# Optimization experiments

Measured on AMD Instinct MI355X. Metric: run time of the kernel, lower is better.

The kernel has to match this reference:

```python
import jax, jax.numpy as jnp
import numpy as np

START_LABEL_ID = 4  # tag_to_ix['[CLS]']


def setup_inputs() -> dict:
    key = jax.random.key(0)
    k1, k2 = jax.random.split(key)
    B, T, K = 256, 4096, 6
    feats = jax.random.normal(k1, (B, T, K), dtype=jnp.float32)
    transitions = jax.random.normal(k2, (B, T, K, K), dtype=jnp.float32)
    return {"feats": feats, "transitions": transitions}


def reference(feats, transitions):
    # Viterbi decode (Bert_BiLSTM_CRF._viterbi_decode):
    #   log_delta init -10000 except start tag; per step t:
    #     scores   = transitions[:, t] + log_delta[:, None, :]   # [B, K, K]
    #     log_delta = max_k scores + feats[:, t]
    #     psi[:, t] = argmax_k scores  (backpointers)
    B, T, K = feats.shape
    init = jnp.full((B, K), -10000.0, dtype=feats.dtype).at[:, START_LABEL_ID].set(0.0)

    def step(delta, xs):
        trans_t, feat_t = xs                       # [B,K,K], [B,K]
        scores = trans_t + delta[:, None, :]       # [B,K,K]
        new_delta = jnp.max(scores, axis=-1) + feat_t
        psi_t = jnp.argmax(scores, axis=-1)        # [B,K] backpointers
        return new_delta, psi_t

    # time-major xs for scan over t = 1..T-1
    xs = (jnp.swapaxes(transitions[:, 1:], 0, 1),  # [T-1,B,K,K]
          jnp.swapaxes(feats[:, 1:], 0, 1))        # [T-1,B,K]
    final_delta, psis = jax.lax.scan(step, init, xs)  # psis: [T-1,B,K]

    score = jnp.max(final_delta, axis=-1)              # [B]
    last_tag = jnp.argmax(final_delta, axis=-1)        # [B]

    # Backtrack: path[t] = psi[t+1][path[t+1]]; psis[i] is psi at time i+1,
    # so path[t] = gather(psis[t], path[t+1]) for t = T-2 .. 0.
    def back(next_tag, psi_t):
        tag = jnp.take_along_axis(psi_t, next_tag[:, None], axis=-1)[:, 0]
        return tag, tag

    _, tags = jax.lax.scan(back, last_tag, psis, reverse=True)  # tags[i] = path[i], i=0..T-2
    path = jnp.concatenate([tags, last_tag[None, :]], axis=0).T  # [B,T]
    return score, path
```

## Files before the change

### kernel.cpp

```cpp
#include <hip/hip_runtime.h>

#define NB 256
#define NT 4096
#define CH 128
#define NCHUNK (NT / CH)

typedef unsigned int u32;
typedef unsigned long long u64;
typedef int v2i __attribute__((ext_vector_type(2)));

typedef __attribute__((address_space(1))) const u32 gas_u32;
typedef __attribute__((address_space(3))) u32 las_u32;

__device__ __forceinline__ void gll16(const void* g, void* l) {
  __builtin_amdgcn_global_load_lds((gas_u32*)g, (las_u32*)l, 16, 0, 0);
}

template <int CTRL>
__device__ __forceinline__ float dppf(float x) {
  return __int_as_float(__builtin_amdgcn_update_dpp(
      0, __float_as_int(x), CTRL, 0xF, 0xF, true));
}

__device__ __forceinline__ float pl16max(float x) {
#if __has_builtin(__builtin_amdgcn_permlane16_swap)
  v2i r = __builtin_amdgcn_permlane16_swap(__float_as_int(x), __float_as_int(x),
                                           false, false);
  return fmaxf(__int_as_float(r[0]), __int_as_float(r[1]));
#else
  return fmaxf(x, __shfl_xor(x, 16, 64));
#endif
}

__device__ __forceinline__ float pl32max(float x) {
#if __has_builtin(__builtin_amdgcn_permlane32_swap)
  v2i r = __builtin_amdgcn_permlane32_swap(__float_as_int(x), __float_as_int(x),
                                           false, false);
  return fmaxf(__int_as_float(r[0]), __int_as_float(r[1]));
#else
  return fmaxf(x, __shfl_xor(x, 32, 64));
#endif
}

__global__ void __launch_bounds__(64, 1)
viterbi_k(const float* __restrict__ feats, const float* __restrict__ trans,
          float* __restrict__ out) {
  __shared__ __align__(16) float s_tr[2 * CH * 36];
  __shared__ __align__(16) float s_ft[2 * CH * 6];
  __shared__ u32 s_psi[NT];
  __shared__ u32 s_path[NT / 4];

  const int b = blockIdx.x;
  const int lane = (int)threadIdx.x;
  const int g = lane >> 3;
  const int l = lane & 7;
  const int gg = (g < 6) ? g : 5;
  const int jj = (l < 6) ? l : 5;
  const int offTA = gg * 6 + jj;
  const int offTB = jj * 6 + gg;
  const int offFA = gg;
  const int offFB = jj;

  const float* trb = trans + (size_t)b * NT * 36;
  const float* ftb = feats + (size_t)b * NT * 6;

  float delta = (l == 4) ? 0.0f : -10000.0f;
  u32 mlo = 0, mhi = 0;

  auto stage = [&](int c) {
    const int buf = c & 1;
    const float* gt = trb + (size_t)c * CH * 36;
    float* lt = s_tr + buf * (CH * 36);
#pragma unroll
    for (int i = 0; i < 18; ++i) gll16(gt + i * 256 + lane * 4, lt + i * 256);
    const float* gf = ftb + (size_t)c * CH * 6;
    float* lf = s_ft + buf * (CH * 6);
#pragma unroll
    for (int i = 0; i < 3; ++i) gll16(gf + i * 256 + lane * 4, lf + i * 256);
  };

  auto stepA = [&](float tr, float ft, int slot) {
    float s = tr + delta;
    float m = fmaxf(s, dppf<0xB1>(s));
    m = fmaxf(m, dppf<0x4E>(m));
    m = fmaxf(m, dppf<0x141>(m));
    u64 bal = __ballot(s == m);
    bool cap = (lane == slot);
    mlo = cap ? (u32)bal : mlo;
    mhi = cap ? (u32)(bal >> 32) : mhi;
    delta = m + ft;
  };

  auto stepB = [&](float tr, float ft, int slot) {
    float s = tr + delta;
    float m = fmaxf(s, dppf<0x128>(s));
    m = pl16max(m);
    m = pl32max(m);
    u64 bal = __ballot(s == m);
    bool cap = (lane == slot);
    mlo = cap ? (u32)bal : mlo;
    mhi = cap ? (u32)(bal >> 32) : mhi;
    delta = m + ft;
  };

  auto flush = [&](int base) {
    const u32 ub = (u32)(base >> 6) & 63;
    u32 pA = (u32)__builtin_ctz((mlo & 63u) | 64u);
    pA |= (u32)__builtin_ctz(((mlo >> 8) & 63u) | 64u) << 3;
    pA |= (u32)__builtin_ctz(((mlo >> 16) & 63u) | 64u) << 6;
    pA |= (u32)__builtin_ctz(((mlo >> 24) & 63u) | 64u) << 9;
    pA |= (u32)__builtin_ctz((mhi & 63u) | 64u) << 12;
    pA |= (u32)__builtin_ctz(((mhi >> 8) & 63u) | 64u) << 15;
    u64 bal = ((u64)mhi << 32) | (u64)mlo;
    u32 pB = 0;
#pragma unroll
    for (int i = 0; i < 6; ++i) {
      u64 mm = (bal >> i) & 0x0000010101010101ULL;
      u32 j = (u32)(__builtin_ctzll(mm | (1ULL << 48)) >> 3);
      pB |= j << (3 * i);
    }
    u32 p = (lane & 1) ? pA : pB;
    s_psi[base + (((u32)lane) ^ ub)] = p;
  };

#define LOAD8(trv, ftv, g8base)                                               \
  {                                                                           \
    _Pragma("unroll") for (int q = 0; q < 8; ++q) {                           \
      trv[q] = trp[((g8base) + q) * 36 + ((q & 1) ? offTA : offTB)];          \
      ftv[q] = ftp[((g8base) + q) * 6 + ((q & 1) ? offFA : offFB)];           \
    }                                                                         \
  }

#define STEPS8(trv, ftv, base)                                                \
  {                                                                           \
    _Pragma("unroll") for (int q = 0; q < 8; ++q) {                           \
      if (q & 1) stepA(trv[q], ftv[q], ((base) + q) & 63);                    \
      else       stepB(trv[q], ftv[q], ((base) + q) & 63);                    \
    }                                                                         \
  }

  stage(0);
  asm volatile("s_waitcnt vmcnt(0)" ::: "memory");
  stage(1);

  {
    const float* trp = s_tr;
    const float* ftp = s_ft;
    float trA[8], ftA[8], trB[8], ftB[8];
    LOAD8(trA, ftA, 0);
    LOAD8(trB, ftB, 8);
#pragma unroll
    for (int q = 1; q < 8; ++q) {
      if (q & 1) stepA(trA[q], ftA[q], q);
      else       stepB(trA[q], ftA[q], q);
    }
    LOAD8(trA, ftA, 16);
    STEPS8(trB, ftB, 8);
#pragma unroll 1
    for (int g2 = 2; g2 < 16; g2 += 2) {
      LOAD8(trB, ftB, (g2 + 1) * 8);
      STEPS8(trA, ftA, g2 * 8);
      LOAD8(trA, ftA, (g2 + 2) * 8);
      STEPS8(trB, ftB, (g2 + 1) * 8);
      if ((g2 & 7) == 6) flush((g2 & 8) * 8);
    }
  }

#pragma unroll 1
  for (int c = 1; c < NCHUNK; ++c) {
    asm volatile("s_waitcnt vmcnt(0)" ::: "memory");
    if (c + 1 < NCHUNK) stage(c + 1);
    const int buf = c & 1;
    const float* trp = s_tr + buf * (CH * 36);
    const float* ftp = s_ft + buf * (CH * 6);
    const int tbase = c * CH;
    float trA[8], ftA[8], trB[8], ftB[8];
    LOAD8(trA, ftA, 0);
#pragma unroll 1
    for (int g2 = 0; g2 < 16; g2 += 2) {
      LOAD8(trB, ftB, (g2 + 1) * 8);
      STEPS8(trA, ftA, tbase + g2 * 8);
      LOAD8(trA, ftA, (g2 + 2) * 8);
      STEPS8(trB, ftB, tbase + (g2 + 1) * 8);
      if ((g2 & 7) == 6) flush(tbase + (g2 & 8) * 8);
    }
  }

  float sm = delta;
  sm = fmaxf(sm, dppf<0xB1>(sm));
  sm = fmaxf(sm, dppf<0x4E>(sm));
  sm = fmaxf(sm, dppf<0x141>(sm));
  sm = fmaxf(sm, dppf<0x128>(sm));
  sm = pl16max(sm);
  sm = pl32max(sm);
  u64 bs = __ballot(delta == sm);
  int last_tag = (int)((__builtin_ctzll(bs) >> 3) & 7);

  __syncthreads();

  const int u = lane;
  u32 Gm = 0u | (1u << 3) | (2u << 6) | (3u << 9) | (4u << 12) | (5u << 15);
#pragma unroll 1
  for (int k = 0; k < 64; ++k) {
    u32 p = s_psi[u * 64 + (k ^ u)];
    u32 ng = 0;
#pragma unroll
    for (int x = 0; x < 6; ++x) {
      u32 j = (p >> (3 * x)) & 7;
      u32 v = (Gm >> (3 * ((j < 6) ? j : 0))) & 7;
      ng |= v << (3 * x);
    }
    Gm = ng;
  }

  int bcur = last_tag;
  int my_b = last_tag;
#pragma unroll 1
  for (int v = 63; v >= 1; --v) {
    u32 Gv = (u32)__builtin_amdgcn_readlane((int)Gm, v);
    bcur = (int)((Gv >> (3 * bcur)) & 7);
    my_b = (u == v - 1) ? bcur : my_b;
  }

  {
    int tag = my_b;
    unsigned char* pb = (unsigned char*)s_path;
    pb[u * 64 + 63] = (unsigned char)tag;
#pragma unroll 1
    for (int k = 63; k >= 1; --k) {
      u32 p = s_psi[u * 64 + (k ^ u)];
      tag = (int)((p >> (3 * tag)) & 7);
      pb[u * 64 + k - 1] = (unsigned char)tag;
    }
  }
  if (lane == 0) out[b] = sm;
  __syncthreads();

  float* outp = out + NB + (size_t)b * NT;
#pragma unroll
  for (int i = 0; i < (NT / 4) / 64; ++i) {
    u32 w = s_path[lane + i * 64];
    float4 f;
    f.x = (float)(w & 255u);
    f.y = (float)((w >> 8) & 255u);
    f.z = (float)((w >> 16) & 255u);
    f.w = (float)((w >> 24) & 255u);
    ((float4*)outp)[lane + i * 64] = f;
  }
}

extern "C" void kernel_launch(void* const* d_in, const int* in_sizes, int n_in,
                              void* d_out, int out_size, void* d_ws, size_t ws_size,
                              hipStream_t stream) {
  (void)in_sizes; (void)n_in; (void)out_size; (void)d_ws; (void)ws_size;
  const float* feats = (const float*)d_in[0];
  const float* trans = (const float*)d_in[1];
  float* out = (float*)d_out;
  hipLaunchKernelGGL(viterbi_k, dim3(NB), dim3(64), 0, stream, feats, trans, out);
}
```

Measured before the change: 242.2 us.

## Interleave two batch rows per wavefront to hide serial Viterbi latency

Each 64-lane block now processes two batch rows and interleaves their dependent max/argmax chains, so one chain's cross-lane DPP, permlane and ballot latency can overlap with the other's. The staging chunk shrinks from 128 to 32 steps, and the LDS buffers are doubled to hold both rows. The grid is halved to 128 blocks, which on a 256-CU part leaves about half the CUs idle. Backtracking runs once per row, one after the other.

```diff
diff --git a/kernel.cpp b/kernel.cpp
--- a/kernel.cpp
+++ b/kernel.cpp
@@ -2,7 +2,7 @@
 
 #define NB 256
 #define NT 4096
-#define CH 128
+#define CH 32
 #define NCHUNK (NT / CH)
 
 typedef unsigned int u32;
@@ -45,12 +45,11 @@
 __global__ void __launch_bounds__(64, 1)
 viterbi_k(const float* __restrict__ feats, const float* __restrict__ trans,
           float* __restrict__ out) {
-  __shared__ __align__(16) float s_tr[2 * CH * 36];
-  __shared__ __align__(16) float s_ft[2 * CH * 6];
-  __shared__ u32 s_psi[NT];
+  __shared__ __align__(16) float s_tr[2 * 2 * CH * 36];
+  __shared__ __align__(16) float s_ft[2 * 2 * CH * 6];
+  __shared__ u32 s_psi[2 * NT];
   __shared__ u32 s_path[NT / 4];
 
-  const int b = blockIdx.x;
   const int lane = (int)threadIdx.x;
   const int g = lane >> 3;
   const int l = lane & 7;
@@ -61,49 +60,71 @@
   const int offFA = gg;
   const int offFB = jj;
 
-  const float* trb = trans + (size_t)b * NT * 36;
-  const float* ftb = feats + (size_t)b * NT * 6;
-
-  float delta = (l == 4) ? 0.0f : -10000.0f;
-  u32 mlo = 0, mhi = 0;
+  const int b0 = blockIdx.x * 2, b1 = b0 + 1;
+  const float* trb0 = trans + (size_t)b0 * NT * 36;
+  const float* ftb0 = feats + (size_t)b0 * NT * 6;
+  const float* trb1 = trans + (size_t)b1 * NT * 36;
+  const float* ftb1 = feats + (size_t)b1 * NT * 6;
+
+  float d0 = (l == 4) ? 0.0f : -10000.0f;
+  float d1 = d0;
+  u32 mlo0 = 0, mhi0 = 0, mlo1 = 0, mhi1 = 0;
 
   auto stage = [&](int c) {
     const int buf = c & 1;
-    const float* gt = trb + (size_t)c * CH * 36;
-    float* lt = s_tr + buf * (CH * 36);
-#pragma unroll
-    for (int i = 0; i < 18; ++i) gll16(gt + i * 256 + lane * 4, lt + i * 256);
-    const float* gf = ftb + (size_t)c * CH * 6;
-    float* lf = s_ft + buf * (CH * 6);
-#pragma unroll
-    for (int i = 0; i < 3; ++i) gll16(gf + i * 256 + lane * 4, lf + i * 256);
+    {
+      const float* gt = trb0 + (size_t)c * (CH * 36);
+      float* lt = s_tr + buf * (CH * 36);
+#pragma unroll
+      for (int i = 0; i < 4; ++i) gll16(gt + i * 256 + lane * 4, lt + i * 256);
+      if (lane < 32) gll16(gt + 1024 + lane * 4, lt + 1024);
+      const float* gf = ftb0 + (size_t)c * (CH * 6);
+      float* lf = s_ft + buf * (CH * 6);
+      if (lane < 48) gll16(gf + lane * 4, lf);
+    }
+    {
+      const float* gt = trb1 + (size_t)c * (CH * 36);
+      float* lt = s_tr + 2 * (CH * 36) + buf * (CH * 36);
+#pragma unroll
+      for (int i = 0; i < 4; ++i) gll16(gt + i * 256 + lane * 4, lt + i * 256);
+      if (lane < 32) gll16(gt + 1024 + lane * 4, lt + 1024);
+      const float* gf = ftb1 + (size_t)c * (CH * 6);
+      float* lf = s_ft + 2 * (CH * 6) + buf * (CH * 6);
+      if (lane < 48) gll16(gf + lane * 4, lf);
+    }
   };
 
-  auto stepA = [&](float tr, float ft, int slot) {
-    float s = tr + delta;
-    float m = fmaxf(s, dppf<0xB1>(s));
-    m = fmaxf(m, dppf<0x4E>(m));
-    m = fmaxf(m, dppf<0x141>(m));
-    u64 bal = __ballot(s == m);
+  auto stepA2 = [&](float t0, float f0, float t1, float f1, int slot) {
+    float s0 = t0 + d0, s1 = t1 + d1;
+    float m0 = fmaxf(s0, dppf<0xB1>(s0));
+    float m1 = fmaxf(s1, dppf<0xB1>(s1));
+    m0 = fmaxf(m0, dppf<0x4E>(m0));
+    m1 = fmaxf(m1, dppf<0x4E>(m1));
+    m0 = fmaxf(m0, dppf<0x141>(m0));
+    m1 = fmaxf(m1, dppf<0x141>(m1));
+    u64 a0 = __ballot(s0 == m0);
+    u64 a1 = __ballot(s1 == m1);
     bool cap = (lane == slot);
-    mlo = cap ? (u32)bal : mlo;
-    mhi = cap ? (u32)(bal >> 32) : mhi;
-    delta = m + ft;
+    mlo0 = cap ? (u32)a0 : mlo0;  mhi0 = cap ? (u32)(a0 >> 32) : mhi0;
+    mlo1 = cap ? (u32)a1 : mlo1;  mhi1 = cap ? (u32)(a1 >> 32) : mhi1;
+    d0 = m0 + f0;  d1 = m1 + f1;
   };
 
-  auto stepB = [&](float tr, float ft, int slot) {
-    float s = tr + delta;
-    float m = fmaxf(s, dppf<0x128>(s));
-    m = pl16max(m);
-    m = pl32max(m);
-    u64 bal = __ballot(s == m);
+  auto stepB2 = [&](float t0, float f0, float t1, float f1, int slot) {
+    float s0 = t0 + d0, s1 = t1 + d1;
+    float m0 = fmaxf(s0, dppf<0x128>(s0));
+    float m1 = fmaxf(s1, dppf<0x128>(s1));
+    m0 = pl16max(m0);  m1 = pl16max(m1);
+    m0 = pl32max(m0);  m1 = pl32max(m1);
+    u64 a0 = __ballot(s0 == m0);
+    u64 a1 = __ballot(s1 == m1);
     bool cap = (lane == slot);
-    mlo = cap ? (u32)bal : mlo;
-    mhi = cap ? (u32)(bal >> 32) : mhi;
-    delta = m + ft;
+    mlo0 = cap ? (u32)a0 : mlo0;  mhi0 = cap ? (u32)(a0 >> 32) : mhi0;
+    mlo1 = cap ? (u32)a1 : mlo1;  mhi1 = cap ? (u32)(a1 >> 32) : mhi1;
+    d0 = m0 + f0;  d1 = m1 + f1;
   };
 
-  auto flush = [&](int base) {
+  auto flushOne = [&](int base, u32 mlo, u32 mhi, u32* psib) {
     const u32 ub = (u32)(base >> 6) & 63;
     u32 pA = (u32)__builtin_ctz((mlo & 63u) | 64u);
     pA |= (u32)__builtin_ctz(((mlo >> 8) & 63u) | 64u) << 3;
@@ -120,22 +141,36 @@
       pB |= j << (3 * i);
     }
     u32 p = (lane & 1) ? pA : pB;
-    s_psi[base + (((u32)lane) ^ ub)] = p;
+    psib[base + (((u32)lane) ^ ub)] = p;
   };
 
-#define LOAD8(trv, ftv, g8base)                                               \
+#define LOAD8x2(T0, F0, T1, F1, g8)                                           \
   {                                                                           \
     _Pragma("unroll") for (int q = 0; q < 8; ++q) {                           \
-      trv[q] = trp[((g8base) + q) * 36 + ((q & 1) ? offTA : offTB)];          \
-      ftv[q] = ftp[((g8base) + q) * 6 + ((q & 1) ? offFA : offFB)];           \
+      T0[q] = trp0[((g8) + q) * 36 + ((q & 1) ? offTA : offTB)];              \
+      F0[q] = ftp0[((g8) + q) * 6 + ((q & 1) ? offFA : offFB)];               \
+      T1[q] = trp1[((g8) + q) * 36 + ((q & 1) ? offTA : offTB)];              \
+      F1[q] = ftp1[((g8) + q) * 6 + ((q & 1) ? offFA : offFB)];               \
     }                                                                         \
   }
 
-#define STEPS8(trv, ftv, base)                                                \
+#define STEPS8x2(T0, F0, T1, F1, SB)                                          \
   {                                                                           \
     _Pragma("unroll") for (int q = 0; q < 8; ++q) {                           \
-      if (q & 1) stepA(trv[q], ftv[q], ((base) + q) & 63);                    \
-      else       stepB(trv[q], ftv[q], ((base) + q) & 63);                    \
+      if (q & 1) stepA2(T0[q], F0[q], T1[q], F1[q], (SB) + q);                \
+      else       stepB2(T0[q], F0[q], T1[q], F1[q], (SB) + q);                \
+    }                                                                         \
+  }
+
+#define STEPS8Lx2(T0, F0, T1, F1, SB, N0, G0, N1, G1, ng8)                    \
+  {                                                                           \
+    _Pragma("unroll") for (int q = 0; q < 8; ++q) {                           \
+      if (q & 1) stepA2(T0[q], F0[q], T1[q], F1[q], (SB) + q);                \
+      else       stepB2(T0[q], F0[q], T1[q], F1[q], (SB) + q);                \
+      N0[q] = trp0[((ng8) + q) * 36 + ((q & 1) ? offTA : offTB)];             \
+      G0[q] = ftp0[((ng8) + q) * 6 + ((q & 1) ? offFA : offFB)];              \
+      N1[q] = trp1[((ng8) + q) * 36 + ((q & 1) ? offTA : offTB)];             \
+      G1[q] = ftp1[((ng8) + q) * 6 + ((q & 1) ? offFA : offFB)];              \
     }                                                                         \
   }
 
@@ -144,26 +179,21 @@
   stage(1);
 
   {
-    const float* trp = s_tr;
-    const float* ftp = s_ft;
-    float trA[8], ftA[8], trB[8], ftB[8];
-    LOAD8(trA, ftA, 0);
-    LOAD8(trB, ftB, 8);
+    const float* trp0 = s_tr;
+    const float* ftp0 = s_ft;
+    const float* trp1 = s_tr + 2 * (CH * 36);
+    const float* ftp1 = s_ft + 2 * (CH * 6);
+    float tA0[8], fA0[8], tA1[8], fA1[8], tB0[8], fB0[8], tB1[8], fB1[8];
+    LOAD8x2(tA0, fA0, tA1, fA1, 0);
+    LOAD8x2(tB0, fB0, tB1, fB1, 8);
 #pragma unroll
     for (int q = 1; q < 8; ++q) {
-      if (q & 1) stepA(trA[q], ftA[q], q);
-      else       stepB(trA[q], ftA[q], q);
-    }
-    LOAD8(trA, ftA, 16);
-    STEPS8(trB, ftB, 8);
-#pragma unroll 1
-    for (int g2 = 2; g2 < 16; g2 += 2) {
-      LOAD8(trB, ftB, (g2 + 1) * 8);
-      STEPS8(trA, ftA, g2 * 8);
-      LOAD8(trA, ftA, (g2 + 2) * 8);
-      STEPS8(trB, ftB, (g2 + 1) * 8);
-      if ((g2 & 7) == 6) flush((g2 & 8) * 8);
-    }
+      if (q & 1) stepA2(tA0[q], fA0[q], tA1[q], fA1[q], q);
+      else       stepB2(tA0[q], fA0[q], tA1[q], fA1[q], q);
+    }
+    STEPS8Lx2(tB0, fB0, tB1, fB1, 8, tA0, fA0, tA1, fA1, 16);
+    STEPS8Lx2(tA0, fA0, tA1, fA1, 16, tB0, fB0, tB1, fB1, 24);
+    STEPS8x2(tB0, fB0, tB1, fB1, 24);
   }
 
 #pragma unroll 1
@@ -171,81 +201,106 @@
     asm volatile("s_waitcnt vmcnt(0)" ::: "memory");
     if (c + 1 < NCHUNK) stage(c + 1);
     const int buf = c & 1;
-    const float* trp = s_tr + buf * (CH * 36);
-    const float* ftp = s_ft + buf * (CH * 6);
-    const int tbase = c * CH;
-    float trA[8], ftA[8], trB[8], ftB[8];
-    LOAD8(trA, ftA, 0);
-#pragma unroll 1
-    for (int g2 = 0; g2 < 16; g2 += 2) {
-      LOAD8(trB, ftB, (g2 + 1) * 8);
-      STEPS8(trA, ftA, tbase + g2 * 8);
-      LOAD8(trA, ftA, (g2 + 2) * 8);
-      STEPS8(trB, ftB, tbase + (g2 + 1) * 8);
-      if ((g2 & 7) == 6) flush(tbase + (g2 & 8) * 8);
-    }
-  }
-
-  float sm = delta;
-  sm = fmaxf(sm, dppf<0xB1>(sm));
-  sm = fmaxf(sm, dppf<0x4E>(sm));
-  sm = fmaxf(sm, dppf<0x141>(sm));
-  sm = fmaxf(sm, dppf<0x128>(sm));
-  sm = pl16max(sm);
-  sm = pl32max(sm);
-  u64 bs = __ballot(delta == sm);
-  int last_tag = (int)((__builtin_ctzll(bs) >> 3) & 7);
-
-  __syncthreads();
+    const float* trp0 = s_tr + buf * (CH * 36);
+    const float* ftp0 = s_ft + buf * (CH * 6);
+    const float* trp1 = s_tr + 2 * (CH * 36) + buf * (CH * 36);
+    const float* ftp1 = s_ft + 2 * (CH * 6) + buf * (CH * 6);
+    const int sb = (c & 1) * 32;
+    float tA0[8], fA0[8], tA1[8], fA1[8], tB0[8], fB0[8], tB1[8], fB1[8];
+    LOAD8x2(tA0, fA0, tA1, fA1, 0);
+    STEPS8Lx2(tA0, fA0, tA1, fA1, sb, tB0, fB0, tB1, fB1, 8);
+    STEPS8Lx2(tB0, fB0, tB1, fB1, sb + 8, tA0, fA0, tA1, fA1, 16);
+    STEPS8Lx2(tA0, fA0, tA1, fA1, sb + 16, tB0, fB0, tB1, fB1, 24);
+    STEPS8x2(tB0, fB0, tB1, fB1, sb + 24);
+    if (c & 1) {
+      const int base = (c >> 1) * 64;
+      flushOne(base, mlo0, mhi0, s_psi);
+      flushOne(base, mlo1, mhi1, s_psi + NT);
+    }
+  }
+
+  float sm0, sm1;
+  int last0, last1;
+  {
+    float sm = d0;
+    sm = fmaxf(sm, dppf<0xB1>(sm));
+    sm = fmaxf(sm, dppf<0x4E>(sm));
+    sm = fmaxf(sm, dppf<0x141>(sm));
+    sm = fmaxf(sm, dppf<0x128>(sm));
+    sm = pl16max(sm);
+    sm = pl32max(sm);
+    u64 bs = __ballot(d0 == sm);
+    last0 = (int)((__builtin_ctzll(bs) >> 3) & 7);
+    sm0 = sm;
+  }
+  {
+    float sm = d1;
+    sm = fmaxf(sm, dppf<0xB1>(sm));
+    sm = fmaxf(sm, dppf<0x4E>(sm));
+    sm = fmaxf(sm, dppf<0x141>(sm));
+    sm = fmaxf(sm, dppf<0x128>(sm));
+    sm = pl16max(sm);
+    sm = pl32max(sm);
+    u64 bs = __ballot(d1 == sm);
+    last1 = (int)((__builtin_ctzll(bs) >> 3) & 7);
+    sm1 = sm;
+  }
+  if (lane == 0) { out[b0] = sm0; out[b1] = sm1; }
 
   const int u = lane;
-  u32 Gm = 0u | (1u << 3) | (2u << 6) | (3u << 9) | (4u << 12) | (5u << 15);
-#pragma unroll 1
-  for (int k = 0; k < 64; ++k) {
-    u32 p = s_psi[u * 64 + (k ^ u)];
-    u32 ng = 0;
-#pragma unroll
-    for (int x = 0; x < 6; ++x) {
-      u32 j = (p >> (3 * x)) & 7;
-      u32 v = (Gm >> (3 * ((j < 6) ? j : 0))) & 7;
-      ng |= v << (3 * x);
-    }
-    Gm = ng;
-  }
-
-  int bcur = last_tag;
-  int my_b = last_tag;
-#pragma unroll 1
-  for (int v = 63; v >= 1; --v) {
-    u32 Gv = (u32)__builtin_amdgcn_readlane((int)Gm, v);
-    bcur = (int)((Gv >> (3 * bcur)) & 7);
-    my_b = (u == v - 1) ? bcur : my_b;
-  }
-
-  {
-    int tag = my_b;
-    unsigned char* pb = (unsigned char*)s_path;
-    pb[u * 64 + 63] = (unsigned char)tag;
-#pragma unroll 1
-    for (int k = 63; k >= 1; --k) {
-      u32 p = s_psi[u * 64 + (k ^ u)];
-      tag = (int)((p >> (3 * tag)) & 7);
-      pb[u * 64 + k - 1] = (unsigned char)tag;
-    }
-  }
-  if (lane == 0) out[b] = sm;
-  __syncthreads();
-
-  float* outp = out + NB + (size_t)b * NT;
-#pragma unroll
-  for (int i = 0; i < (NT / 4) / 64; ++i) {
-    u32 w = s_path[lane + i * 64];
-    float4 f;
-    f.x = (float)(w & 255u);
-    f.y = (float)((w >> 8) & 255u);
-    f.z = (float)((w >> 16) & 255u);
-    f.w = (float)((w >> 24) & 255u);
-    ((float4*)outp)[lane + i * 64] = f;
+#pragma unroll 1
+  for (int bb = 0; bb < 2; ++bb) {
+    u32* psib = s_psi + bb * NT;
+    int last_tag = bb ? last1 : last0;
+    __syncthreads();
+
+    u32 Gm = 0u | (1u << 3) | (2u << 6) | (3u << 9) | (4u << 12) | (5u << 15);
+#pragma unroll 1
+    for (int k = 0; k < 64; ++k) {
+      u32 p = psib[u * 64 + (k ^ u)];
+      u32 ng = 0;
+#pragma unroll
+      for (int x = 0; x < 6; ++x) {
+        u32 j = (p >> (3 * x)) & 7;
+        u32 v = (Gm >> (3 * ((j < 6) ? j : 0))) & 7;
+        ng |= v << (3 * x);
+      }
+      Gm = ng;
+    }
+
+    int bcur = last_tag;
+    int my_b = last_tag;
+#pragma unroll 1
+    for (int v = 63; v >= 1; --v) {
+      u32 Gv = (u32)__builtin_amdgcn_readlane((int)Gm, v);
+      bcur = (int)((Gv >> (3 * bcur)) & 7);
+      my_b = (u == v - 1) ? bcur : my_b;
+    }
+
+    {
+      int tag = my_b;
+      unsigned char* pb = (unsigned char*)s_path;
+      pb[u * 64 + 63] = (unsigned char)tag;
+#pragma unroll 1
+      for (int k = 63; k >= 1; --k) {
+        u32 p = psib[u * 64 + (k ^ u)];
+        tag = (int)((p >> (3 * tag)) & 7);
+        pb[u * 64 + k - 1] = (unsigned char)tag;
+      }
+    }
+    __syncthreads();
+
+    float* outp = out + NB + (size_t)(bb ? b1 : b0) * NT;
+#pragma unroll
+    for (int i = 0; i < (NT / 4) / 64; ++i) {
+      u32 w = s_path[lane + i * 64];
+      float4 f;
+      f.x = (float)(w & 255u);
+      f.y = (float)((w >> 8) & 255u);
+      f.z = (float)((w >> 16) & 255u);
+      f.w = (float)((w >> 24) & 255u);
+      ((float4*)outp)[lane + i * 64] = f;
+    }
   }
 }
 
@@ -256,5 +311,6 @@
   const float* feats = (const float*)d_in[0];
   const float* trans = (const float*)d_in[1];
   float* out = (float*)d_out;
-  hipLaunchKernelGGL(viterbi_k, dim3(NB), dim3(64), 0, stream, feats, trans, out);
-}
+  hipLaunchKernelGGL(viterbi_k, dim3(NB / 2), dim3(64), 0, stream,
+                     feats, trans, out);
+}
```

After: 444.7 us. 83.6% more time.
